# Kernel optimization log

Hardware: AMD Instinct MI355X
Metric: run time of the kernel (lower is better)

## Reference

```python
import jax, jax.numpy as jnp
import numpy as np

EPS = 1e-12  # tf.math.l2_normalize epsilon

def _l2norm(x):
    # normalize over last axis, matching K.l2_normalize semantics
    sq = jnp.sum(x * x, axis=-1, keepdims=True)
    return x * jax.lax.rsqrt(jnp.maximum(sq, EPS))

def setup_inputs() -> dict:
    key = jax.random.key(0)
    k1, k2, k3 = jax.random.split(key, 3)
    B, L, D, P = 16, 256, 256, 20
    sent1 = jax.random.normal(k1, (B, L, D), dtype=jnp.float32)
    sent2 = jax.random.normal(k2, (B, L, D), dtype=jnp.float32)
    # glorot_uniform for shape (P, D)
    limit = np.sqrt(6.0 / (P + D)).astype(np.float32)
    kernel = jax.random.uniform(k3, (P, D), minval=-limit, maxval=limit, dtype=jnp.float32)
    return {"sent1": sent1, "sent2": sent2, "kernel": kernel}

def reference(sent1, sent2, kernel):
    # sent1: [B,L1,D], sent2: [B,L2,D], kernel: [P,D]
    v1 = _l2norm(sent1[:, :, None, :] * kernel)  # [B,L1,P,D]
    v2 = _l2norm(sent2[:, :, None, :] * kernel)  # [B,L2,P,D]
    # per-perspective cosine similarity matrix: [B,L1,L2,P]
    cos = jnp.einsum('blpd,bmpd->blmp', v1, v2)
    # max over the other sentence's positions (L2) -> [B,L1,P]
    return jnp.max(cos, axis=2)
```

## Files before the change

kernel.cpp:

```cpp
#include <hip/hip_runtime.h>
#include <hip/hip_bf16.h>


#define B_DIM 16
#define L_DIM 256
#define D_DIM 256
#define P_DIM 20
#define EPS 1e-12f

typedef __attribute__((ext_vector_type(8))) __bf16 bf16x8;
typedef __attribute__((ext_vector_type(4))) float f32x4;

__device__ __forceinline__ unsigned short f2bf(float x) {
  unsigned int u = __float_as_uint(x);
  u += 0x7fffu + ((u >> 16) & 1u);
  return (unsigned short)(u >> 16);
}

__global__ __launch_bounds__(256)
void prep_kernel(const float* __restrict__ s1, const float* __restrict__ s2,
                 const float* __restrict__ kg, float* __restrict__ rn1,
                 float* __restrict__ rn2, unsigned short* __restrict__ s2bf) {
  const int lane = threadIdx.x & 63;
  const int gw   = blockIdx.x * 4 + (threadIdx.x >> 6);
  const int sent = gw >> 12;
  const int row  = gw & 4095;
  const float* src = sent ? s2 : s1;
  float4 sv = *(const float4*)(src + (size_t)row * D_DIM + lane * 4);
  if (sent) {
    unsigned int p0 = ((unsigned int)f2bf(sv.y) << 16) | f2bf(sv.x);
    unsigned int p1 = ((unsigned int)f2bf(sv.w) << 16) | f2bf(sv.z);
    *(uint2*)&s2bf[(size_t)row * D_DIM + lane * 4] = make_uint2(p0, p1);
  }
  float q0 = sv.x * sv.x, q1 = sv.y * sv.y, q2 = sv.z * sv.z, q3 = sv.w * sv.w;
  float* rn = sent ? rn2 : rn1;
  const int b = row >> 8, l = row & 255;
  #pragma unroll 4
  for (int p = 0; p < P_DIM; ++p) {
    float4 kv = *(const float4*)(kg + p * D_DIM + lane * 4);
    float v = q0 * kv.x * kv.x + q1 * kv.y * kv.y + q2 * kv.z * kv.z + q3 * kv.w * kv.w;
    #pragma unroll
    for (int off = 1; off < 64; off <<= 1) v += __shfl_xor(v, off);
    if (lane == 0) rn[((size_t)b * P_DIM + p) * L_DIM + l] = rsqrtf(fmaxf(v, EPS));
  }
}

__global__ __launch_bounds__(256, 1)
void mpm_main(const float* __restrict__ s1, const unsigned short* __restrict__ s2bf,
              const float* __restrict__ kg, const float* __restrict__ rn1,
              const float* __restrict__ rn2, float* __restrict__ outg) {
  __shared__ __align__(16) unsigned short X2[256 * 256];
  __shared__ __align__(16) unsigned short X1[64 * 256];
  float* WoutF = (float*)X1;

  const int tid  = threadIdx.x;
  const int lane = tid & 63;
  const int wave = tid >> 6;
  const int lr   = lane & 15;
  const int q    = lane >> 4;

  const int bid = blockIdx.x;
  const int pgi = bid & 3;
  const int lt  = (bid >> 2) & 3;
  const int b   = bid >> 4;
  const int l0  = lt * 64;

  {
    const unsigned short* s2b = s2bf + (size_t)b * L_DIM * D_DIM;
    #pragma unroll
    for (int j = 0; j < 32; ++j) {
      int g = j * 256 + tid;
      int r = g >> 5, pr = g & 31;
      int c = pr ^ (r & 31);
      __builtin_amdgcn_global_load_lds(
          (const __attribute__((address_space(1))) void*)(s2b + r * 256 + c * 8),
          (__attribute__((address_space(3))) void*)(X2 + (size_t)g * 8),
          16, 0, 0);
    }
  }

  float4 s1r[16];
  {
    const float* s1b = s1 + ((size_t)b * L_DIM + l0) * D_DIM;
    #pragma unroll
    for (int i = 0; i < 16; ++i)
      s1r[i] = *(const float4*)(s1b + (i * 4 + wave) * D_DIM + lane * 4);
  }

  int mrow[4], mkey[4];
  #pragma unroll
  for (int mi = 0; mi < 4; ++mi) {
    mrow[mi] = wave * 64 + mi * 16 + lr;
    mkey[mi] = mrow[mi] & 31;
  }

  #pragma unroll 1
  for (int pp = 0; pp < 5; ++pp) {
    const int p = pgi * 5 + pp;
    __syncthreads();

    {
      float4 kv = *(const float4*)(kg + p * D_DIM + lane * 4);
      const float k0 = kv.x * kv.x, k1 = kv.y * kv.y, k2 = kv.z * kv.z, k3 = kv.w * kv.w;
      const float* rn1b = rn1 + ((size_t)b * P_DIM + p) * L_DIM + l0;
      #pragma unroll
      for (int i = 0; i < 16; ++i) {
        const int row = i * 4 + wave;
        const float rv = rn1b[row];
        float x0 = s1r[i].x * k0 * rv, x1 = s1r[i].y * k1 * rv;
        float x2 = s1r[i].z * k2 * rv, x3 = s1r[i].w * k3 * rv;
        unsigned int p0 = ((unsigned int)f2bf(x1) << 16) | f2bf(x0);
        unsigned int p1 = ((unsigned int)f2bf(x3) << 16) | f2bf(x2);
        *(uint2*)&X1[row * 256 + (((lane >> 1) ^ (row & 31)) << 3) + ((lane & 1) << 2)] =
            make_uint2(p0, p1);
      }
    }
    __syncthreads();

    f32x4 acc[4][4];
    #pragma unroll
    for (int mi = 0; mi < 4; ++mi)
      #pragma unroll
      for (int li = 0; li < 4; ++li) acc[mi][li] = (f32x4){0.f, 0.f, 0.f, 0.f};

    #pragma unroll
    for (int kstep = 0; kstep < 8; ++kstep) {
      const int cc = kstep * 4 + q;
      bf16x8 a[4], bb[4];
      #pragma unroll
      for (int mi = 0; mi < 4; ++mi)
        a[mi] = *(const bf16x8*)&X2[mrow[mi] * 256 + ((cc ^ mkey[mi]) << 3)];
      #pragma unroll
      for (int li = 0; li < 4; ++li) {
        const int l = li * 16 + lr;
        bb[li] = *(const bf16x8*)&X1[l * 256 + ((cc ^ (l & 31)) << 3)];
      }
      #pragma unroll
      for (int mi = 0; mi < 4; ++mi)
        #pragma unroll
        for (int li = 0; li < 4; ++li)
          acc[mi][li] = __builtin_amdgcn_mfma_f32_16x16x32_bf16(a[mi], bb[li], acc[mi][li], 0, 0, 0);
    }

    float4 r2[4];
    {
      const float* rn2b = rn2 + ((size_t)b * P_DIM + p) * L_DIM + wave * 64;
      #pragma unroll
      for (int mi = 0; mi < 4; ++mi)
        r2[mi] = *(const float4*)(rn2b + mi * 16 + q * 4);
    }
    float v[4];
    #pragma unroll
    for (int li = 0; li < 4; ++li) {
      float t = -3.4e38f;
      #pragma unroll
      for (int mi = 0; mi < 4; ++mi) {
        t = fmaxf(t, acc[mi][li][0] * r2[mi].x);
        t = fmaxf(t, acc[mi][li][1] * r2[mi].y);
        t = fmaxf(t, acc[mi][li][2] * r2[mi].z);
        t = fmaxf(t, acc[mi][li][3] * r2[mi].w);
      }
      t = fmaxf(t, __shfl_xor(t, 16));
      t = fmaxf(t, __shfl_xor(t, 32));
      v[li] = t;
    }

    __syncthreads();
    if (q == 0) {
      #pragma unroll
      for (int li = 0; li < 4; ++li) WoutF[wave * 64 + li * 16 + lr] = v[li];
    }
    __syncthreads();
    if (tid < 64) {
      float o = fmaxf(fmaxf(WoutF[tid], WoutF[64 + tid]),
                      fmaxf(WoutF[128 + tid], WoutF[192 + tid]));
      outg[((size_t)b * L_DIM + (l0 + tid)) * P_DIM + p] = o;
    }
  }
}

extern "C" void kernel_launch(void* const* d_in, const int* in_sizes, int n_in,
                              void* d_out, int out_size, void* d_ws, size_t ws_size,
                              hipStream_t stream) {
  const float* s1 = (const float*)d_in[0];
  const float* s2 = (const float*)d_in[1];
  const float* kg = (const float*)d_in[2];
  float* out = (float*)d_out;

  float* rn1 = (float*)d_ws;
  float* rn2 = rn1 + (size_t)B_DIM * P_DIM * L_DIM;
  unsigned short* s2bf = (unsigned short*)(rn2 + (size_t)B_DIM * P_DIM * L_DIM);

  prep_kernel<<<dim3(2048), dim3(256), 0, stream>>>(s1, s2, kg, rn1, rn2, s2bf);
  mpm_main<<<dim3(256), dim3(256), 0, stream>>>(s1, s2bf, kg, rn1, rn2, out);
}
```

Measured before the change: 96.06 us.

## Compute norms via MFMA in prep, convert s1 to bf16, use 8-wave main blocks

The prep kernel now computes the per-perspective squared norms as a small bf16 MFMA GEMM (squared sentence rows times squared kernel rows) instead of a 64-lane shuffle reduction per perspective. It also writes a bf16 copy of sent1. The main kernel reads the bf16 sent1 (half the register footprint and load traffic) and runs 512 threads, each wave covering 32 rows of sent2, to add latency hiding. Computing the squared terms in bf16 lowers norm precision, and the 8-way final max reduction adds some LDS work.

Measured after the change: 82.60 us. -14.0%, faster.

```diff
diff --git a/kernel.cpp b/kernel.cpp
--- a/kernel.cpp
+++ b/kernel.cpp
@@ -7,6 +7,7 @@
 #define D_DIM 256
 #define P_DIM 20
 #define EPS 1e-12f
+#define LDP 264
 
 typedef __attribute__((ext_vector_type(8))) __bf16 bf16x8;
 typedef __attribute__((ext_vector_type(4))) float f32x4;
@@ -18,81 +19,98 @@
 }
 
 __global__ __launch_bounds__(256)
-void prep_kernel(const float* __restrict__ s1, const float* __restrict__ s2,
-                 const float* __restrict__ kg, float* __restrict__ rn1,
-                 float* __restrict__ rn2, unsigned short* __restrict__ s2bf) {
-  const int lane = threadIdx.x & 63;
-  const int gw   = blockIdx.x * 4 + (threadIdx.x >> 6);
-  const int sent = gw >> 12;
-  const int row  = gw & 4095;
+void prep2(const float* __restrict__ s1, const float* __restrict__ s2,
+           const float* __restrict__ kg,
+           float* __restrict__ rn1, float* __restrict__ rn2,
+           unsigned short* __restrict__ s1bf, unsigned short* __restrict__ s2bf) {
+  __shared__ __align__(16) unsigned short QA[32 * LDP];
+  __shared__ __align__(16) unsigned short QB[32 * LDP];
+  const int tid = threadIdx.x, lane = tid & 63, wave = tid >> 6;
+  const int lr = lane & 15, q = lane >> 4;
+  const int sent = blockIdx.x & 1, t = blockIdx.x >> 1;
+  const int r0 = t * 32, b = r0 >> 8;
   const float* src = sent ? s2 : s1;
-  float4 sv = *(const float4*)(src + (size_t)row * D_DIM + lane * 4);
-  if (sent) {
-    unsigned int p0 = ((unsigned int)f2bf(sv.y) << 16) | f2bf(sv.x);
-    unsigned int p1 = ((unsigned int)f2bf(sv.w) << 16) | f2bf(sv.z);
-    *(uint2*)&s2bf[(size_t)row * D_DIM + lane * 4] = make_uint2(p0, p1);
-  }
-  float q0 = sv.x * sv.x, q1 = sv.y * sv.y, q2 = sv.z * sv.z, q3 = sv.w * sv.w;
+  unsigned short* sbf = sent ? s2bf : s1bf;
   float* rn = sent ? rn2 : rn1;
-  const int b = row >> 8, l = row & 255;
-  #pragma unroll 4
-  for (int p = 0; p < P_DIM; ++p) {
-    float4 kv = *(const float4*)(kg + p * D_DIM + lane * 4);
-    float v = q0 * kv.x * kv.x + q1 * kv.y * kv.y + q2 * kv.z * kv.z + q3 * kv.w * kv.w;
-    #pragma unroll
-    for (int off = 1; off < 64; off <<= 1) v += __shfl_xor(v, off);
-    if (lane == 0) rn[((size_t)b * P_DIM + p) * L_DIM + l] = rsqrtf(fmaxf(v, EPS));
-  }
-}
-
-__global__ __launch_bounds__(256, 1)
-void mpm_main(const float* __restrict__ s1, const unsigned short* __restrict__ s2bf,
+
+  #pragma unroll
+  for (int i = 0; i < 8; ++i) {
+    const int row = i * 4 + wave;
+    float4 sv = *(const float4*)(src + (size_t)(r0 + row) * D_DIM + lane * 4);
+    unsigned int c0 = ((unsigned int)f2bf(sv.y) << 16) | f2bf(sv.x);
+    unsigned int c1 = ((unsigned int)f2bf(sv.w) << 16) | f2bf(sv.z);
+    *(uint2*)&sbf[(size_t)(r0 + row) * D_DIM + lane * 4] = make_uint2(c0, c1);
+    unsigned int q0 = ((unsigned int)f2bf(sv.y * sv.y) << 16) | f2bf(sv.x * sv.x);
+    unsigned int q1 = ((unsigned int)f2bf(sv.w * sv.w) << 16) | f2bf(sv.z * sv.z);
+    *(uint2*)&QA[row * LDP + lane * 4] = make_uint2(q0, q1);
+  }
+  #pragma unroll
+  for (int j = 0; j < 5; ++j) {
+    const int row = wave * 5 + j;
+    float4 kv = *(const float4*)(kg + row * D_DIM + lane * 4);
+    unsigned int c0 = ((unsigned int)f2bf(kv.y * kv.y) << 16) | f2bf(kv.x * kv.x);
+    unsigned int c1 = ((unsigned int)f2bf(kv.w * kv.w) << 16) | f2bf(kv.z * kv.z);
+    *(uint2*)&QB[row * LDP + lane * 4] = make_uint2(c0, c1);
+  }
+  __syncthreads();
+
+  const int mt = wave & 1, nt = wave >> 1;
+  f32x4 acc = {0.f, 0.f, 0.f, 0.f};
+  #pragma unroll
+  for (int ks = 0; ks < 8; ++ks) {
+    const int cc = ks * 4 + q;
+    bf16x8 a  = *(const bf16x8*)&QA[(mt * 16 + lr) * LDP + cc * 8];
+    bf16x8 bb = *(const bf16x8*)&QB[(nt * 16 + lr) * LDP + cc * 8];
+    acc = __builtin_amdgcn_mfma_f32_16x16x32_bf16(a, bb, acc, 0, 0, 0);
+  }
+  const int p = nt * 16 + lr;
+  if (p < P_DIM) {
+    #pragma unroll
+    for (int r = 0; r < 4; ++r) {
+      const int l = (r0 & 255) + mt * 16 + q * 4 + r;
+      rn[((size_t)b * P_DIM + p) * L_DIM + l] = rsqrtf(fmaxf(acc[r], EPS));
+    }
+  }
+}
+
+__global__ __launch_bounds__(512, 1)
+void mpm_main(const unsigned short* __restrict__ s1bf,
+              const unsigned short* __restrict__ s2bf,
               const float* __restrict__ kg, const float* __restrict__ rn1,
               const float* __restrict__ rn2, float* __restrict__ outg) {
   __shared__ __align__(16) unsigned short X2[256 * 256];
   __shared__ __align__(16) unsigned short X1[64 * 256];
   float* WoutF = (float*)X1;
 
-  const int tid  = threadIdx.x;
-  const int lane = tid & 63;
-  const int wave = tid >> 6;
-  const int lr   = lane & 15;
-  const int q    = lane >> 4;
-
+  const int tid = threadIdx.x, lane = tid & 63, wave = tid >> 6;
+  const int lr = lane & 15, q = lane >> 4;
   const int bid = blockIdx.x;
-  const int pgi = bid & 3;
-  const int lt  = (bid >> 2) & 3;
-  const int b   = bid >> 4;
-  const int l0  = lt * 64;
+  const int pgi = bid & 3, lt = (bid >> 2) & 3, b = bid >> 4;
+  const int l0 = lt * 64;
 
   {
     const unsigned short* s2b = s2bf + (size_t)b * L_DIM * D_DIM;
     #pragma unroll
-    for (int j = 0; j < 32; ++j) {
-      int g = j * 256 + tid;
+    for (int j = 0; j < 16; ++j) {
+      int g = j * 512 + tid;
       int r = g >> 5, pr = g & 31;
       int c = pr ^ (r & 31);
       __builtin_amdgcn_global_load_lds(
           (const __attribute__((address_space(1))) void*)(s2b + r * 256 + c * 8),
-          (__attribute__((address_space(3))) void*)(X2 + (size_t)g * 8),
-          16, 0, 0);
-    }
-  }
-
-  float4 s1r[16];
+          (__attribute__((address_space(3))) void*)(X2 + (size_t)g * 8), 16, 0, 0);
+    }
+  }
+
+  uint2 s1r[8];
   {
-    const float* s1b = s1 + ((size_t)b * L_DIM + l0) * D_DIM;
-    #pragma unroll
-    for (int i = 0; i < 16; ++i)
-      s1r[i] = *(const float4*)(s1b + (i * 4 + wave) * D_DIM + lane * 4);
-  }
-
-  int mrow[4], mkey[4];
-  #pragma unroll
-  for (int mi = 0; mi < 4; ++mi) {
-    mrow[mi] = wave * 64 + mi * 16 + lr;
-    mkey[mi] = mrow[mi] & 31;
-  }
+    const unsigned short* s1b = s1bf + ((size_t)b * L_DIM + l0) * D_DIM;
+    #pragma unroll
+    for (int i = 0; i < 8; ++i)
+      s1r[i] = *(const uint2*)(s1b + (size_t)(i * 8 + wave) * D_DIM + lane * 4);
+  }
+
+  const int mrow0 = wave * 32 + lr,  mrow1 = wave * 32 + 16 + lr;
+  const int mkey0 = mrow0 & 31,      mkey1 = mrow1 & 31;
 
   #pragma unroll 1
   for (int pp = 0; pp < 5; ++pp) {
@@ -104,62 +122,59 @@
       const float k0 = kv.x * kv.x, k1 = kv.y * kv.y, k2 = kv.z * kv.z, k3 = kv.w * kv.w;
       const float* rn1b = rn1 + ((size_t)b * P_DIM + p) * L_DIM + l0;
       #pragma unroll
-      for (int i = 0; i < 16; ++i) {
-        const int row = i * 4 + wave;
+      for (int i = 0; i < 8; ++i) {
+        const int row = i * 8 + wave;
         const float rv = rn1b[row];
-        float x0 = s1r[i].x * k0 * rv, x1 = s1r[i].y * k1 * rv;
-        float x2 = s1r[i].z * k2 * rv, x3 = s1r[i].w * k3 * rv;
-        unsigned int p0 = ((unsigned int)f2bf(x1) << 16) | f2bf(x0);
-        unsigned int p1 = ((unsigned int)f2bf(x3) << 16) | f2bf(x2);
+        float x0 = __uint_as_float(s1r[i].x << 16)          * k0 * rv;
+        float x1 = __uint_as_float(s1r[i].x & 0xffff0000u)  * k1 * rv;
+        float x2 = __uint_as_float(s1r[i].y << 16)          * k2 * rv;
+        float x3 = __uint_as_float(s1r[i].y & 0xffff0000u)  * k3 * rv;
+        unsigned int c0 = ((unsigned int)f2bf(x1) << 16) | f2bf(x0);
+        unsigned int c1 = ((unsigned int)f2bf(x3) << 16) | f2bf(x2);
         *(uint2*)&X1[row * 256 + (((lane >> 1) ^ (row & 31)) << 3) + ((lane & 1) << 2)] =
-            make_uint2(p0, p1);
+            make_uint2(c0, c1);
       }
     }
     __syncthreads();
 
-    f32x4 acc[4][4];
-    #pragma unroll
-    for (int mi = 0; mi < 4; ++mi)
+    f32x4 acc[2][4];
+    #pragma unroll
+    for (int mi = 0; mi < 2; ++mi)
       #pragma unroll
       for (int li = 0; li < 4; ++li) acc[mi][li] = (f32x4){0.f, 0.f, 0.f, 0.f};
 
     #pragma unroll
-    for (int kstep = 0; kstep < 8; ++kstep) {
-      const int cc = kstep * 4 + q;
-      bf16x8 a[4], bb[4];
-      #pragma unroll
-      for (int mi = 0; mi < 4; ++mi)
-        a[mi] = *(const bf16x8*)&X2[mrow[mi] * 256 + ((cc ^ mkey[mi]) << 3)];
+    for (int ks = 0; ks < 8; ++ks) {
+      const int cc = ks * 4 + q;
+      bf16x8 a0 = *(const bf16x8*)&X2[mrow0 * 256 + ((cc ^ mkey0) << 3)];
+      bf16x8 a1 = *(const bf16x8*)&X2[mrow1 * 256 + ((cc ^ mkey1) << 3)];
+      bf16x8 bb[4];
       #pragma unroll
       for (int li = 0; li < 4; ++li) {
         const int l = li * 16 + lr;
         bb[li] = *(const bf16x8*)&X1[l * 256 + ((cc ^ (l & 31)) << 3)];
       }
       #pragma unroll
-      for (int mi = 0; mi < 4; ++mi)
-        #pragma unroll
-        for (int li = 0; li < 4; ++li)
-          acc[mi][li] = __builtin_amdgcn_mfma_f32_16x16x32_bf16(a[mi], bb[li], acc[mi][li], 0, 0, 0);
-    }
-
-    float4 r2[4];
+      for (int li = 0; li < 4; ++li) {
+        acc[0][li] = __builtin_amdgcn_mfma_f32_16x16x32_bf16(a0, bb[li], acc[0][li], 0, 0, 0);
+        acc[1][li] = __builtin_amdgcn_mfma_f32_16x16x32_bf16(a1, bb[li], acc[1][li], 0, 0, 0);
+      }
+    }
+
+    float4 r20, r21;
     {
-      const float* rn2b = rn2 + ((size_t)b * P_DIM + p) * L_DIM + wave * 64;
-      #pragma unroll
-      for (int mi = 0; mi < 4; ++mi)
-        r2[mi] = *(const float4*)(rn2b + mi * 16 + q * 4);
+      const float* rn2b = rn2 + ((size_t)b * P_DIM + p) * L_DIM + wave * 32;
+      r20 = *(const float4*)(rn2b + q * 4);
+      r21 = *(const float4*)(rn2b + 16 + q * 4);
     }
     float v[4];
     #pragma unroll
     for (int li = 0; li < 4; ++li) {
       float t = -3.4e38f;
-      #pragma unroll
-      for (int mi = 0; mi < 4; ++mi) {
-        t = fmaxf(t, acc[mi][li][0] * r2[mi].x);
-        t = fmaxf(t, acc[mi][li][1] * r2[mi].y);
-        t = fmaxf(t, acc[mi][li][2] * r2[mi].z);
-        t = fmaxf(t, acc[mi][li][3] * r2[mi].w);
-      }
+      t = fmaxf(t, fmaxf(acc[0][li][0] * r20.x, acc[1][li][0] * r21.x));
+      t = fmaxf(t, fmaxf(acc[0][li][1] * r20.y, acc[1][li][1] * r21.y));
+      t = fmaxf(t, fmaxf(acc[0][li][2] * r20.z, acc[1][li][2] * r21.z));
+      t = fmaxf(t, fmaxf(acc[0][li][3] * r20.w, acc[1][li][3] * r21.w));
       t = fmaxf(t, __shfl_xor(t, 16));
       t = fmaxf(t, __shfl_xor(t, 32));
       v[li] = t;
@@ -172,8 +187,9 @@
     }
     __syncthreads();
     if (tid < 64) {
-      float o = fmaxf(fmaxf(WoutF[tid], WoutF[64 + tid]),
-                      fmaxf(WoutF[128 + tid], WoutF[192 + tid]));
+      float o = WoutF[tid];
+      #pragma unroll
+      for (int w = 1; w < 8; ++w) o = fmaxf(o, WoutF[w * 64 + tid]);
       outg[((size_t)b * L_DIM + (l0 + tid)) * P_DIM + p] = o;
     }
   }
@@ -190,7 +206,8 @@
   float* rn1 = (float*)d_ws;
   float* rn2 = rn1 + (size_t)B_DIM * P_DIM * L_DIM;
   unsigned short* s2bf = (unsigned short*)(rn2 + (size_t)B_DIM * P_DIM * L_DIM);
-
-  prep_kernel<<<dim3(2048), dim3(256), 0, stream>>>(s1, s2, kg, rn1, rn2, s2bf);
-  mpm_main<<<dim3(256), dim3(256), 0, stream>>>(s1, s2bf, kg, rn1, rn2, out);
-}
+  unsigned short* s1bf = s2bf + (size_t)B_DIM * L_DIM * D_DIM;
+
+  prep2<<<dim3(256), dim3(256), 0, stream>>>(s1, s2, kg, rn1, rn2, s1bf, s2bf);
+  mpm_main<<<dim3(256), dim3(512), 0, stream>>>(s1bf, s2bf, kg, rn1, rn2, out);
+}
```
